# Performance work log

Measured on AMD Instinct MI355X. Metric: run time of the kernel, lower is better.

## Reference

```python
import jax, jax.numpy as jnp
import numpy as np
import math

B, S, D, H, WIN = 2, 4096, 512, 8, 50
DK = D // H


def setup_inputs() -> dict:
    key = jax.random.key(0)
    ks = jax.random.split(key, 10)
    scale = 0.02
    return {
        "x": jax.random.normal(ks[0], (B, S, D), dtype=jnp.float32),
        "opcode_types": jax.random.randint(ks[1], (B, S), 0, 10, dtype=jnp.int64),
        "Wq": jax.random.normal(ks[2], (D, D), dtype=jnp.float32) * scale,
        "bq": jnp.zeros((D,), dtype=jnp.float32),
        "Wk": jax.random.normal(ks[3], (D, D), dtype=jnp.float32) * scale,
        "bk": jnp.zeros((D,), dtype=jnp.float32),
        "Wv": jax.random.normal(ks[4], (D, D), dtype=jnp.float32) * scale,
        "bv": jnp.zeros((D,), dtype=jnp.float32),
        "Wo": jax.random.normal(ks[5], (D, D), dtype=jnp.float32) * scale,
        "bo": jnp.zeros((D,), dtype=jnp.float32),
    }


def reference(x, opcode_types, Wq, bq, Wk, bk, Wv, bv, Wo, bo):
    b, s, d = x.shape
    # Linear projections (torch Linear: x @ W.T + b), split heads -> [B,H,S,DK]
    q = (x @ Wq.T + bq).reshape(b, s, H, DK).transpose(0, 2, 1, 3)
    k = (x @ Wk.T + bk).reshape(b, s, H, DK).transpose(0, 2, 1, 3)
    v = (x @ Wv.T + bv).reshape(b, s, H, DK).transpose(0, 2, 1, 3)

    pos = jnp.arange(s)
    window = jnp.abs(pos[:, None] - pos[None, :]) <= WIN          # [S,S]
    ctrl_cols = (opcode_types == 0).any(axis=0)                   # [S]
    allow = window | ctrl_cols[None, :]                           # [S,S]

    scores = jnp.einsum("bhqd,bhkd->bhqk", q, k) / math.sqrt(DK)  # [B,H,S,S]
    scores = jnp.where(allow[None, None], scores, jnp.float32(-1e9))
    attn = jax.nn.softmax(scores, axis=-1)
    attn = jnp.nan_to_num(attn, nan=0.0)
    out = jnp.einsum("bhqk,bhkd->bhqd", attn, v)                  # [B,H,S,DK]
    out = out.transpose(0, 2, 1, 3).reshape(b, s, d)
    return out @ Wo.T + bo
```

## Files before the change

### kernel.cpp

```cpp
#include <hip/hip_runtime.h>
#include <hip/hip_bf16.h>
#include <math.h>

#define B_ 2
#define S_ 4096
#define D_ 512
#define H_ 8
#define DK_ 64
#define WIN_ 50
#define NGT 32

typedef __attribute__((ext_vector_type(8))) short short8;
typedef __attribute__((ext_vector_type(4))) float f32x4;
typedef __attribute__((ext_vector_type(4))) unsigned short us4;
typedef unsigned short ushort_t;

__device__ __forceinline__ unsigned short f2bf(float f) {
    unsigned u = __builtin_bit_cast(unsigned, f);
    u += 0x7FFF + ((u >> 16) & 1);
    return (unsigned short)(u >> 16);
}
__device__ __forceinline__ float bf2f(unsigned short h) {
    return __builtin_bit_cast(float, ((unsigned)h) << 16);
}
__device__ __forceinline__ unsigned pack_bf16(float lo, float hi) {
    return ((unsigned)f2bf(hi) << 16) | (unsigned)f2bf(lo);
}

__global__ __launch_bounds__(1024) void build_glist(const int* __restrict__ opcode,
                                                    int* __restrict__ glist,
                                                    int* __restrict__ gcount) {
    __shared__ int cnts[1024];
    int t = threadIdx.x;
    int f[4]; int c = 0;
    for (int k = 0; k < 4; ++k) {
        int col = t * 4 + k;
        int flag = 0;
        for (int b = 0; b < B_; ++b) flag |= (opcode[b * S_ + col] == 0) ? 1 : 0;
        f[k] = flag; c += flag;
    }
    cnts[t] = c;
    __syncthreads();
    for (int off = 1; off < 1024; off <<= 1) {
        int v = cnts[t];
        int add = (t >= off) ? cnts[t - off] : 0;
        __syncthreads();
        cnts[t] = v + add;
        __syncthreads();
    }
    int base = cnts[t] - c;
    for (int k = 0; k < 4; ++k) {
        if (f[k]) glist[base++] = t * 4 + k;
    }
    if (t == 1023) gcount[0] = cnts[1023];
}

__global__ __launch_bounds__(256) void split_x(const float* __restrict__ src,
                                               ushort_t* __restrict__ hi,
                                               ushort_t* __restrict__ lo) {
    int i = blockIdx.x * 256 + threadIdx.x;
    f32x4 v = ((const f32x4*)src)[i];
    us4 h, l;
    for (int e = 0; e < 4; ++e) {
        unsigned short hb = f2bf(v[e]);
        h[e] = hb;
        l[e] = f2bf(v[e] - bf2f(hb));
    }
    ((us4*)hi)[i] = h;
    ((us4*)lo)[i] = l;
}

__global__ __launch_bounds__(256) void split_w4(const float* __restrict__ W0, const float* __restrict__ W1,
                                                const float* __restrict__ W2, const float* __restrict__ W3,
                                                ushort_t* __restrict__ H0, ushort_t* __restrict__ H1,
                                                ushort_t* __restrict__ H2, ushort_t* __restrict__ H3,
                                                ushort_t* __restrict__ L0, ushort_t* __restrict__ L1,
                                                ushort_t* __restrict__ L2, ushort_t* __restrict__ L3) {
    const float* src; ushort_t* hp; ushort_t* lp;
    switch (blockIdx.y) {
        case 0: src = W0; hp = H0; lp = L0; break;
        case 1: src = W1; hp = H1; lp = L1; break;
        case 2: src = W2; hp = H2; lp = L2; break;
        default: src = W3; hp = H3; lp = L3; break;
    }
    int i = blockIdx.x * 256 + threadIdx.x;
    f32x4 v = ((const f32x4*)src)[i];
    us4 h, l;
    for (int e = 0; e < 4; ++e) {
        unsigned short hb = f2bf(v[e]);
        h[e] = hb;
        l[e] = f2bf(v[e] - bf2f(hb));
    }
    ((us4*)hp)[i] = h;
    ((us4*)lp)[i] = l;
}

__device__ __forceinline__ void gemm_epi(f32x4 (&acc)[4][4], const float* __restrict__ bias,
                                         void* __restrict__ outp, int mode, float scale,
                                         int m0, int n0, int t) {
    const int lane = t & 63, wave = t >> 6;
    const int lrow = lane & 15, lkg = lane >> 4;
    const int wr = wave >> 1, wc = wave & 1;
    for (int m = 0; m < 4; ++m)
        for (int n = 0; n < 4; ++n) {
            int col = n0 + wc * 64 + n * 16 + lrow;
            int row_base = m0 + wr * 64 + m * 16 + lkg * 4;
            float bs = bias[col];
            float vv[4];
            for (int r = 0; r < 4; ++r) vv[r] = (acc[m][n][r] + bs) * scale;
            if (mode == 0) {
                for (int r = 0; r < 4; ++r)
                    ((float*)outp)[(size_t)(row_base + r) * D_ + col] = vv[r];
            } else if (mode == 1) {
                int bb = row_base >> 12, s0 = row_base & (S_ - 1);
                int hh = col >> 6, dk = col & 63;
                for (int r = 0; r < 4; ++r)
                    ((ushort_t*)outp)[(((size_t)(bb * H_ + hh) * S_) + s0 + r) * DK_ + dk] = f2bf(vv[r]);
            } else if (mode == 2) {
                int bb = row_base >> 12, s0 = row_base & (S_ - 1);
                int hh = col >> 6, dk = col & 63;
                for (int r = 0; r < 4; ++r) {
                    int s = s0 + r, jt = s >> 6, jr = s & 63;
                    char* img = (char*)outp + (((size_t)(bb * H_ + hh)) * 64 + jt) * 16384;
                    *(ushort_t*)(img + ((jr * 128 + dk * 2) ^ ((jr & 7) << 4))) = f2bf(vv[r]);
                }
            } else {
                int bb = row_base >> 12, s0 = row_base & (S_ - 1);
                int hh = col >> 6, dk = col & 63;
                int jt = s0 >> 6, jr0 = s0 & 63;
                char* img = (char*)outp + (((size_t)(bb * H_ + hh)) * 64 + jt) * 16384 + 8192;
                us4 pk;
                for (int r = 0; r < 4; ++r) pk[r] = f2bf(vv[r]);
                *(us4*)(img + ((dk * 128 + jr0 * 2) ^ ((dk & 7) << 4))) = pk;
            }
        }
}

__device__ __forceinline__ void gemm_core1(const ushort_t* __restrict__ A,
                                           const ushort_t* __restrict__ Bw,
                                           ushort_t (&LDS)[2][8192],
                                           int m0, int n0, int t,
                                           f32x4 (&acc)[4][4]) {
    const int lane = t & 63, wave = t >> 6;
    const int lrow = lane & 15, lkg = lane >> 4;
    const int wr = wave >> 1, wc = wave & 1;
    const ushort_t* srcs[2] = {A, Bw};
    const int row0[2] = {m0, n0};

    auto stage = [&](int buf, int k0) {
        #pragma unroll
        for (int it = 0; it < 4; ++it) {
            int c = it * 4 + wave;
            int tile = c >> 3;
            int kg = (c >> 1) & 3;
            int r = ((c & 1) << 6) | lane;
            const ushort_t* g = srcs[tile] + (size_t)(row0[tile] + r) * 512 + k0 + kg * 8;
            __builtin_amdgcn_global_load_lds(
                (const __attribute__((address_space(1))) void*)g,
                (__attribute__((address_space(3))) void*)(&LDS[buf][c * 512]),
                16, 0, 0);
        }
    };

    stage(0, 0);
    __syncthreads();

    const int aoff = lkg * 1024 + (wr * 64 + lrow) * 8;
    const int boff = 4096 + lkg * 1024 + (wc * 64 + lrow) * 8;
    int cur = 0;
    for (int ks = 0; ks < 16; ++ks) {
        if (ks < 15) stage(cur ^ 1, (ks + 1) * 32);
        const ushort_t* Lb = LDS[cur];
        short8 ah[4], bh[4];
        #pragma unroll
        for (int m = 0; m < 4; ++m) ah[m] = *(const short8*)(Lb + aoff + m * 128);
        #pragma unroll
        for (int n = 0; n < 4; ++n) bh[n] = *(const short8*)(Lb + boff + n * 128);
        #pragma unroll
        for (int m = 0; m < 4; ++m)
            #pragma unroll
            for (int n = 0; n < 4; ++n)
                acc[m][n] = __builtin_amdgcn_mfma_f32_16x16x32_bf16(ah[m], bh[n], acc[m][n], 0, 0, 0);
        __syncthreads();
        cur ^= 1;
    }
}

__device__ __forceinline__ void gemm_core3(const ushort_t* __restrict__ Ah,
                                           const ushort_t* __restrict__ Al,
                                           const ushort_t* __restrict__ Bh,
                                           const ushort_t* __restrict__ Bl,
                                           ushort_t (&LDS)[2][16384],
                                           int m0, int n0, int t,
                                           f32x4 (&acc)[4][4]) {
    const int lane = t & 63, wave = t >> 6;
    const int lrow = lane & 15, lkg = lane >> 4;
    const int wr = wave >> 1, wc = wave & 1;
    const ushort_t* srcs[4] = {Ah, Al, Bh, Bl};
    const int row0[4] = {m0, m0, n0, n0};

    auto stage = [&](int buf, int k0) {
        #pragma unroll
        for (int it = 0; it < 8; ++it) {
            int c = it * 4 + wave;
            int tile = c >> 3;
            int kg = (c >> 1) & 3;
            int r = ((c & 1) << 6) | lane;
            const ushort_t* g = srcs[tile] + (size_t)(row0[tile] + r) * 512 + k0 + kg * 8;
            __builtin_amdgcn_global_load_lds(
                (const __attribute__((address_space(1))) void*)g,
                (__attribute__((address_space(3))) void*)(&LDS[buf][c * 512]),
                16, 0, 0);
        }
    };

    stage(0, 0);
    __syncthreads();

    const int aoff = lkg * 1024 + (wr * 64 + lrow) * 8;
    const int boff = 2 * 4096 + lkg * 1024 + (wc * 64 + lrow) * 8;
    int cur = 0;
    for (int ks = 0; ks < 16; ++ks) {
        if (ks < 15) stage(cur ^ 1, (ks + 1) * 32);
        const ushort_t* Lb = LDS[cur];
        short8 ah[4], al[4], bh[4], bl[4];
        #pragma unroll
        for (int m = 0; m < 4; ++m) {
            ah[m] = *(const short8*)(Lb + aoff + m * 128);
            al[m] = *(const short8*)(Lb + 4096 + aoff + m * 128);
        }
        #pragma unroll
        for (int n = 0; n < 4; ++n) {
            bh[n] = *(const short8*)(Lb + boff + n * 128);
            bl[n] = *(const short8*)(Lb + 4096 + boff + n * 128);
        }
        #pragma unroll
        for (int m = 0; m < 4; ++m)
            #pragma unroll
            for (int n = 0; n < 4; ++n) {
                acc[m][n] = __builtin_amdgcn_mfma_f32_16x16x32_bf16(ah[m], bh[n], acc[m][n], 0, 0, 0);
                acc[m][n] = __builtin_amdgcn_mfma_f32_16x16x32_bf16(al[m], bh[n], acc[m][n], 0, 0, 0);
                acc[m][n] = __builtin_amdgcn_mfma_f32_16x16x32_bf16(ah[m], bl[n], acc[m][n], 0, 0, 0);
            }
        __syncthreads();
        cur ^= 1;
    }
}

__global__ __launch_bounds__(256) void gemm_qkv(const ushort_t* __restrict__ xh,
                                                const ushort_t* __restrict__ whb,
                                                const float* __restrict__ bq,
                                                const float* __restrict__ bk,
                                                const float* __restrict__ bv,
                                                ushort_t* __restrict__ qb,
                                                char* __restrict__ bandimg) {
    __shared__ ushort_t LDS[2][8192];
    int z = blockIdx.z;
    const ushort_t* Bh = whb + (size_t)z * D_ * D_;
    const float* bias = (z == 0) ? bq : (z == 1) ? bk : bv;
    int mode = z + 1;
    float scale = (z == 0) ? 0.125f : 1.0f;
    void* outp = (z == 0) ? (void*)qb : (void*)bandimg;
    f32x4 acc[4][4];
    for (int m = 0; m < 4; ++m)
        for (int n = 0; n < 4; ++n)
            acc[m][n] = f32x4{0.f, 0.f, 0.f, 0.f};
    gemm_core1(xh, Bh, LDS, blockIdx.y * 128, blockIdx.x * 128, threadIdx.x, acc);
    gemm_epi(acc, bias, outp, mode, scale, blockIdx.y * 128, blockIdx.x * 128, threadIdx.x);
}

__global__ __launch_bounds__(256) void gemm_fin(const ushort_t* __restrict__ Ah,
                                                const ushort_t* __restrict__ Al,
                                                const ushort_t* __restrict__ Bh,
                                                const ushort_t* __restrict__ Bl,
                                                const float* __restrict__ bias,
                                                float* __restrict__ outp) {
    __shared__ ushort_t LDS[2][16384];
    f32x4 acc[4][4];
    for (int m = 0; m < 4; ++m)
        for (int n = 0; n < 4; ++n)
            acc[m][n] = f32x4{0.f, 0.f, 0.f, 0.f};
    gemm_core3(Ah, Al, Bh, Bl, LDS, blockIdx.y * 128, blockIdx.x * 128, threadIdx.x, acc);
    gemm_epi(acc, bias, (void*)outp, 0, 1.0f, blockIdx.y * 128, blockIdx.x * 128, threadIdx.x);
}

__global__ __launch_bounds__(256) void prep_glob(const char* __restrict__ bandimg,
                                                 char* __restrict__ globimg,
                                                 const int* __restrict__ glist,
                                                 const int* __restrict__ gcount) {
    int G = gcount[0];
    int gc = blockIdx.x;
    if (gc * 64 >= G) return;
    int h = blockIdx.y, b = blockIdx.z;
    int t = threadIdx.x;
    __shared__ int jl[64];
    if (t < 64) { int gi = gc * 64 + t; jl[t] = (gi < G) ? glist[gi] : -1; }
    __syncthreads();
    const size_t bh = (size_t)(b * H_ + h);
    char* dst = globimg + (bh * NGT + gc) * 16384;
    {
        int c = t >> 2, q = t & 3;
        int jj = jl[c];
        #pragma unroll
        for (int p = 0; p < 2; ++p) {
            int o_dst = c * 128 + q * 32 + p * 16;
            short8 val;
            if (jj >= 0) {
                int jr = jj & 63, jt = jj >> 6;
                const char* src = bandimg + (bh * 64 + jt) * 16384;
                val = *(const short8*)(src + ((jr * 128 + q * 32 + p * 16) ^ ((jr & 7) << 4)));
            } else {
                for (int e = 0; e < 8; ++e) val[e] = 0;
            }
            *(short8*)(dst + (o_dst ^ ((c & 7) << 4))) = val;
        }
    }
    {
        int d = t >> 2, qq = t & 3;
        short8 v0, v1;
        #pragma unroll 16
        for (int i = 0; i < 16; ++i) {
            int c = qq * 16 + i;
            int jj = jl[c];
            ushort_t val = 0;
            if (jj >= 0) {
                int jr = jj & 63, jt = jj >> 6;
                const char* src = bandimg + (bh * 64 + jt) * 16384 + 8192;
                val = *(const ushort_t*)(src + ((d * 128 + jr * 2) ^ ((d & 7) << 4)));
            }
            if (i < 8) v0[i] = val; else v1[i - 8] = val;
        }
        int o = d * 128 + qq * 32;
        *(short8*)(dst + 8192 + (o ^ ((d & 7) << 4))) = v0;
        *(short8*)(dst + 8192 + ((o + 16) ^ ((d & 7) << 4))) = v1;
    }
}

__global__ __launch_bounds__(512) void attn_mfma3(const ushort_t* __restrict__ Qp,
                                                  const char* __restrict__ bandimg,
                                                  const char* __restrict__ globimg,
                                                  const int* __restrict__ glist,
                                                  const int* __restrict__ gcount,
                                                  ushort_t* __restrict__ AOh,
                                                  ushort_t* __restrict__ AOl) {
    __shared__ char buf[2][16384];
    __shared__ int jl[2][64];
    __shared__ ushort_t Ps[8 * 16 * 64];

    const int t = threadIdx.x, lane = t & 63, wave = t >> 6;
    const int q = lane & 15, g = lane >> 4;
    const int i0 = blockIdx.x * 128, h = blockIdx.y, b = blockIdx.z;
    const size_t headoff = ((size_t)(b * H_ + h)) * S_ * DK_;
    const int iq = i0 + wave * 16 + q;

    short8 qa[2];
    {
        const ushort_t* qrow = Qp + headoff + (size_t)iq * DK_;
        qa[0] = *(const short8*)(qrow + 8 * g);
        qa[1] = *(const short8*)(qrow + 32 + 8 * g);
    }

    f32x4 Oa[4];
    for (int n = 0; n < 4; ++n) Oa[n] = f32x4{0.f, 0.f, 0.f, 0.f};
    float m_st = -1e30f, l_st = 0.f;

    int jlo = i0 - WIN_;
    int jt_lo = (jlo < 0) ? 0 : (jlo >> 6);
    int jhi = i0 + 127 + WIN_; if (jhi > S_ - 1) jhi = S_ - 1;
    int jt_hi = jhi >> 6;
    int nband = jt_hi - jt_lo + 1;
    const int G = gcount[0];
    int nglob = (G + 63) >> 6; if (nglob > NGT) nglob = NGT;
    int nchunk = nband + nglob;

    const size_t bh = (size_t)(b * H_ + h);

    auto stage = [&](int ch, int nb) {
        const char* img = (ch < nband)
            ? bandimg + (bh * 64 + (jt_lo + ch)) * 16384
            : globimg + (bh * NGT + (ch - nband)) * 16384;
        #pragma unroll
        for (int i = 0; i < 2; ++i) {
            int seg = wave * 2 + i;
            __builtin_amdgcn_global_load_lds(
                (const __attribute__((address_space(1))) void*)(img + seg * 1024 + lane * 16),
                (__attribute__((address_space(3))) void*)(buf[nb] + seg * 1024),
                16, 0, 0);
        }
        if (t < 64) {
            int j;
            if (ch < nband) j = (jt_lo + ch) * 64 + t;
            else { int gi = (ch - nband) * 64 + t; j = (gi < G) ? glist[gi] : -1; }
            jl[nb][t] = j;
        }
    };

    stage(0, 0);
    __syncthreads();

    int cur = 0;
    for (int ch = 0; ch < nchunk; ++ch) {
        if (ch + 1 < nchunk) stage(ch + 1, cur ^ 1);
        const bool isband = ch < nband;
        const char* Kb = buf[cur];
        const char* Vb = buf[cur] + 8192;

        f32x4 sc[4];
        for (int n = 0; n < 4; ++n) sc[n] = f32x4{0.f, 0.f, 0.f, 0.f};
        #pragma unroll
        for (int n = 0; n < 4; ++n) {
            int row = n * 16 + q;
            #pragma unroll
            for (int kt = 0; kt < 2; ++kt) {
                int kb = (row * 128 + g * 16 + kt * 64) ^ ((row & 7) << 4);
                short8 ka = *(const short8*)(Kb + kb);
                sc[n] = __builtin_amdgcn_mfma_f32_16x16x32_bf16(ka, qa[kt], sc[n], 0, 0, 0);
            }
        }

        float pm = -1e30f;
        #pragma unroll
        for (int n = 0; n < 4; ++n) {
            int4 J = *(const int4*)(&jl[cur][n * 16 + g * 4]);
            int js[4] = {J.x, J.y, J.z, J.w};
            #pragma unroll
            for (int r = 0; r < 4; ++r) {
                int jj = js[r];
                int ad = iq - jj; ad = ad < 0 ? -ad : ad;
                bool allow = (jj >= 0) && (isband ? (ad <= WIN_) : (ad > WIN_));
                float s = allow ? sc[n][r] : -1e30f;
                sc[n][r] = s;
                pm = fmaxf(pm, s);
            }
        }
        pm = fmaxf(pm, __shfl_xor(pm, 16, 64));
        pm = fmaxf(pm, __shfl_xor(pm, 32, 64));

        bool skip = __all(pm <= m_st);
        float fac = 1.0f;
        if (!skip) {
            float mn = fmaxf(m_st, pm);
            fac = __expf(m_st - mn);
            m_st = mn;
        }
        float rs = 0.f;
        #pragma unroll
        for (int n = 0; n < 4; ++n)
            #pragma unroll
            for (int r = 0; r < 4; ++r) {
                float p = __expf(sc[n][r] - m_st);
                sc[n][r] = p;
                rs += p;
            }
        rs += __shfl_xor(rs, 16, 64);
        rs += __shfl_xor(rs, 32, 64);
        l_st = skip ? (l_st + rs) : (l_st * fac + rs);

        ushort_t* Pw = Ps + wave * 1024;
        #pragma unroll
        for (int n = 0; n < 4; ++n)
            #pragma unroll
            for (int hh = 0; hh < 2; ++hh) {
                unsigned pk = pack_bf16(sc[n][2 * hh], sc[n][2 * hh + 1]);
                int off = (q * 128 + n * 32 + g * 8 + hh * 4) ^ ((q & 7) << 4);
                *(unsigned*)((char*)Pw + off) = pk;
            }

        if (!skip) {
            #pragma unroll
            for (int n = 0; n < 4; ++n)
                #pragma unroll
                for (int r = 0; r < 4; ++r) Oa[n][r] *= fac;
        }

        short8 pa[2];
        #pragma unroll
        for (int kt = 0; kt < 2; ++kt) {
            int pb = (q * 128 + g * 16 + kt * 64) ^ ((q & 7) << 4);
            pa[kt] = *(const short8*)((char*)Pw + pb);
        }
        #pragma unroll
        for (int n = 0; n < 4; ++n) {
            int row = n * 16 + q;
            #pragma unroll
            for (int kt = 0; kt < 2; ++kt) {
                int vb = (row * 128 + g * 16 + kt * 64) ^ ((row & 7) << 4);
                short8 va = *(const short8*)(Vb + vb);
                Oa[n] = __builtin_amdgcn_mfma_f32_16x16x32_bf16(va, pa[kt], Oa[n], 0, 0, 0);
            }
        }
        __syncthreads();
        cur ^= 1;
    }

    float inv = 1.0f / l_st;
    #pragma unroll
    for (int n = 0; n < 4; ++n) {
        us4 ph, pl;
        #pragma unroll
        for (int r = 0; r < 4; ++r) {
            float v = Oa[n][r] * inv;
            unsigned short hb = f2bf(v);
            ph[r] = hb;
            pl[r] = f2bf(v - bf2f(hb));
        }
        size_t base = ((size_t)b * S_ + iq) * D_ + h * DK_ + (n * 16 + g * 4);
        *(us4*)(AOh + base) = ph;
        *(us4*)(AOl + base) = pl;
    }
}

extern "C" void kernel_launch(void* const* d_in, const int* in_sizes, int n_in,
                              void* d_out, int out_size, void* d_ws, size_t ws_size,
                              hipStream_t stream) {
    const float* x      = (const float*)d_in[0];
    const int*   opcode = (const int*)d_in[1];
    const float* Wq = (const float*)d_in[2];
    const float* bq = (const float*)d_in[3];
    const float* Wk = (const float*)d_in[4];
    const float* bk = (const float*)d_in[5];
    const float* Wv = (const float*)d_in[6];
    const float* bv = (const float*)d_in[7];
    const float* Wo = (const float*)d_in[8];
    const float* bo = (const float*)d_in[9];
    float* out = (float*)d_out;

    char* ws = (char*)d_ws;
    const size_t bsd = (size_t)B_ * S_ * D_;
    const size_t bf_bytes = bsd * sizeof(ushort_t);
    const size_t w_bytes  = (size_t)D_ * D_ * sizeof(ushort_t);

    ushort_t* qb = (ushort_t*)(ws);
    ushort_t* xh = (ushort_t*)(ws + bf_bytes);
    ushort_t* xl = (ushort_t*)(ws + 2 * bf_bytes);
    ushort_t* aoh = xh;
    ushort_t* aol = xl;
    char* wbase = ws + 3 * bf_bytes;
    ushort_t* Wh[4]; ushort_t* Wl[4];
    for (int i = 0; i < 4; ++i) {
        Wh[i] = (ushort_t*)(wbase + i * w_bytes);
        Wl[i] = (ushort_t*)(wbase + (4 + i) * w_bytes);
    }
    char* bandimg = wbase + 8 * w_bytes;
    char* globimg = bandimg + (size_t)16 * 64 * 16384;
    int* glist  = (int*)(globimg + (size_t)16 * NGT * 16384);
    int* gcount = glist + S_;

    build_glist<<<1, 1024, 0, stream>>>(opcode, glist, gcount);
    split_x<<<(int)(bsd / 4 / 256), 256, 0, stream>>>(x, xh, xl);
    split_w4<<<dim3(D_ * D_ / 4 / 256, 4), 256, 0, stream>>>(Wq, Wk, Wv, Wo,
        Wh[0], Wh[1], Wh[2], Wh[3], Wl[0], Wl[1], Wl[2], Wl[3]);

    gemm_qkv<<<dim3(D_ / 128, (B_ * S_) / 128, 3), 256, 0, stream>>>(
        xh, Wh[0], bq, bk, bv, qb, bandimg);

    prep_glob<<<dim3(NGT, H_, B_), 256, 0, stream>>>(bandimg, globimg, glist, gcount);

    attn_mfma3<<<dim3(S_ / 128, H_, B_), 512, 0, stream>>>(
        qb, bandimg, globimg, glist, gcount, aoh, aol);

    gemm_fin<<<dim3(D_ / 128, (B_ * S_) / 128), 256, 0, stream>>>(
        aoh, aol, Wh[3], Wl[3], bo, out);
}
```

Baseline: 218.5 us.

## Fuse prep kernels, transpose GEMM epilogues, use exp2 softmax and precomputed LDS offsets

Three preprocessing kernels (glist build, x split, weight split) merge into one launch, and the unused x-lo and Q/K/V-lo splits are dropped. The Q and K GEMMs and the output GEMM are transposed (weights as the A operand) so the epilogues write vectorized us4/f32x4 stores. Q is prescaled by log2(e)/8 so attention can use exp2f. The attention kernel precomputes swizzled LDS offsets, computes band masks arithmetically instead of loading a j-list, and packs P with v_cvt_pk_bf16. The aim is to cut launch overhead, preprocessing traffic and ALU work, at the cost of more code complexity and possible epilogue layout bugs.

```diff
diff --git a/kernel.cpp b/kernel.cpp
--- a/kernel.cpp
+++ b/kernel.cpp
@@ -9,6 +9,7 @@
 #define DK_ 64
 #define WIN_ 50
 #define NGT 32
+#define QSCALE 0.18033688011112042f
 
 typedef __attribute__((ext_vector_type(8))) short short8;
 typedef __attribute__((ext_vector_type(4))) float f32x4;
@@ -23,117 +24,67 @@
 __device__ __forceinline__ float bf2f(unsigned short h) {
     return __builtin_bit_cast(float, ((unsigned)h) << 16);
 }
-__device__ __forceinline__ unsigned pack_bf16(float lo, float hi) {
-    return ((unsigned)f2bf(hi) << 16) | (unsigned)f2bf(lo);
-}
-
-__global__ __launch_bounds__(1024) void build_glist(const int* __restrict__ opcode,
-                                                    int* __restrict__ glist,
-                                                    int* __restrict__ gcount) {
-    __shared__ int cnts[1024];
-    int t = threadIdx.x;
-    int f[4]; int c = 0;
-    for (int k = 0; k < 4; ++k) {
-        int col = t * 4 + k;
-        int flag = 0;
-        for (int b = 0; b < B_; ++b) flag |= (opcode[b * S_ + col] == 0) ? 1 : 0;
-        f[k] = flag; c += flag;
-    }
-    cnts[t] = c;
-    __syncthreads();
-    for (int off = 1; off < 1024; off <<= 1) {
-        int v = cnts[t];
-        int add = (t >= off) ? cnts[t - off] : 0;
+__device__ __forceinline__ unsigned cvt_pk_bf16(float lo, float hi) {
+    unsigned r;
+    asm("v_cvt_pk_bf16_f32 %0, %1, %2" : "=v"(r) : "v"(lo), "v"(hi));
+    return r;
+}
+
+__global__ __launch_bounds__(256) void prep_all(const float* __restrict__ x,
+                                                const float* __restrict__ W0,
+                                                const float* __restrict__ W1,
+                                                const float* __restrict__ W2,
+                                                const float* __restrict__ W3,
+                                                const int* __restrict__ opcode,
+                                                ushort_t* __restrict__ xh,
+                                                ushort_t* __restrict__ whb,
+                                                ushort_t* __restrict__ wol,
+                                                int* __restrict__ glist,
+                                                int* __restrict__ gcount) {
+    const int bid = blockIdx.x;
+    const int t = threadIdx.x;
+    if (bid < 4096) {
+        int i = bid * 256 + t;
+        f32x4 v = ((const f32x4*)x)[i];
+        us4 hv;
+        for (int e = 0; e < 4; ++e) hv[e] = f2bf(v[e]);
+        ((us4*)xh)[i] = hv;
+    } else if (bid < 5120) {
+        int b2 = bid - 4096;
+        int wz = b2 >> 8, inner = b2 & 255;
+        const float* src = (wz == 0) ? W0 : (wz == 1) ? W1 : (wz == 2) ? W2 : W3;
+        int i = inner * 256 + t;
+        f32x4 v = ((const f32x4*)src)[i];
+        us4 hv, lv;
+        for (int e = 0; e < 4; ++e) {
+            unsigned short hb = f2bf(v[e]);
+            hv[e] = hb;
+            lv[e] = f2bf(v[e] - bf2f(hb));
+        }
+        ((us4*)(whb + (size_t)wz * D_ * D_))[i] = hv;
+        if (wz == 3) ((us4*)wol)[i] = lv;
+    } else {
+        __shared__ int cnts[256];
+        unsigned fl = 0; int c = 0;
+        for (int k = 0; k < 16; ++k) {
+            int col = t * 16 + k;
+            int flag = (opcode[col] == 0) | (opcode[S_ + col] == 0);
+            fl |= (unsigned)flag << k; c += flag;
+        }
+        cnts[t] = c;
         __syncthreads();
-        cnts[t] = v + add;
-        __syncthreads();
-    }
-    int base = cnts[t] - c;
-    for (int k = 0; k < 4; ++k) {
-        if (f[k]) glist[base++] = t * 4 + k;
-    }
-    if (t == 1023) gcount[0] = cnts[1023];
-}
-
-__global__ __launch_bounds__(256) void split_x(const float* __restrict__ src,
-                                               ushort_t* __restrict__ hi,
-                                               ushort_t* __restrict__ lo) {
-    int i = blockIdx.x * 256 + threadIdx.x;
-    f32x4 v = ((const f32x4*)src)[i];
-    us4 h, l;
-    for (int e = 0; e < 4; ++e) {
-        unsigned short hb = f2bf(v[e]);
-        h[e] = hb;
-        l[e] = f2bf(v[e] - bf2f(hb));
-    }
-    ((us4*)hi)[i] = h;
-    ((us4*)lo)[i] = l;
-}
-
-__global__ __launch_bounds__(256) void split_w4(const float* __restrict__ W0, const float* __restrict__ W1,
-                                                const float* __restrict__ W2, const float* __restrict__ W3,
-                                                ushort_t* __restrict__ H0, ushort_t* __restrict__ H1,
-                                                ushort_t* __restrict__ H2, ushort_t* __restrict__ H3,
-                                                ushort_t* __restrict__ L0, ushort_t* __restrict__ L1,
-                                                ushort_t* __restrict__ L2, ushort_t* __restrict__ L3) {
-    const float* src; ushort_t* hp; ushort_t* lp;
-    switch (blockIdx.y) {
-        case 0: src = W0; hp = H0; lp = L0; break;
-        case 1: src = W1; hp = H1; lp = L1; break;
-        case 2: src = W2; hp = H2; lp = L2; break;
-        default: src = W3; hp = H3; lp = L3; break;
-    }
-    int i = blockIdx.x * 256 + threadIdx.x;
-    f32x4 v = ((const f32x4*)src)[i];
-    us4 h, l;
-    for (int e = 0; e < 4; ++e) {
-        unsigned short hb = f2bf(v[e]);
-        h[e] = hb;
-        l[e] = f2bf(v[e] - bf2f(hb));
-    }
-    ((us4*)hp)[i] = h;
-    ((us4*)lp)[i] = l;
-}
-
-__device__ __forceinline__ void gemm_epi(f32x4 (&acc)[4][4], const float* __restrict__ bias,
-                                         void* __restrict__ outp, int mode, float scale,
-                                         int m0, int n0, int t) {
-    const int lane = t & 63, wave = t >> 6;
-    const int lrow = lane & 15, lkg = lane >> 4;
-    const int wr = wave >> 1, wc = wave & 1;
-    for (int m = 0; m < 4; ++m)
-        for (int n = 0; n < 4; ++n) {
-            int col = n0 + wc * 64 + n * 16 + lrow;
-            int row_base = m0 + wr * 64 + m * 16 + lkg * 4;
-            float bs = bias[col];
-            float vv[4];
-            for (int r = 0; r < 4; ++r) vv[r] = (acc[m][n][r] + bs) * scale;
-            if (mode == 0) {
-                for (int r = 0; r < 4; ++r)
-                    ((float*)outp)[(size_t)(row_base + r) * D_ + col] = vv[r];
-            } else if (mode == 1) {
-                int bb = row_base >> 12, s0 = row_base & (S_ - 1);
-                int hh = col >> 6, dk = col & 63;
-                for (int r = 0; r < 4; ++r)
-                    ((ushort_t*)outp)[(((size_t)(bb * H_ + hh) * S_) + s0 + r) * DK_ + dk] = f2bf(vv[r]);
-            } else if (mode == 2) {
-                int bb = row_base >> 12, s0 = row_base & (S_ - 1);
-                int hh = col >> 6, dk = col & 63;
-                for (int r = 0; r < 4; ++r) {
-                    int s = s0 + r, jt = s >> 6, jr = s & 63;
-                    char* img = (char*)outp + (((size_t)(bb * H_ + hh)) * 64 + jt) * 16384;
-                    *(ushort_t*)(img + ((jr * 128 + dk * 2) ^ ((jr & 7) << 4))) = f2bf(vv[r]);
-                }
-            } else {
-                int bb = row_base >> 12, s0 = row_base & (S_ - 1);
-                int hh = col >> 6, dk = col & 63;
-                int jt = s0 >> 6, jr0 = s0 & 63;
-                char* img = (char*)outp + (((size_t)(bb * H_ + hh)) * 64 + jt) * 16384 + 8192;
-                us4 pk;
-                for (int r = 0; r < 4; ++r) pk[r] = f2bf(vv[r]);
-                *(us4*)(img + ((dk * 128 + jr0 * 2) ^ ((dk & 7) << 4))) = pk;
-            }
-        }
+        for (int off = 1; off < 256; off <<= 1) {
+            int v = cnts[t];
+            int a = (t >= off) ? cnts[t - off] : 0;
+            __syncthreads();
+            cnts[t] = v + a;
+            __syncthreads();
+        }
+        int base = cnts[t] - c;
+        for (int k = 0; k < 16; ++k)
+            if ((fl >> k) & 1) glist[base++] = t * 16 + k;
+        if (t == 255) gcount[0] = cnts[255];
+    }
 }
 
 __device__ __forceinline__ void gemm_core1(const ushort_t* __restrict__ A,
@@ -255,33 +206,90 @@
                                                 ushort_t* __restrict__ qb,
                                                 char* __restrict__ bandimg) {
     __shared__ ushort_t LDS[2][8192];
-    int z = blockIdx.z;
-    const ushort_t* Bh = whb + (size_t)z * D_ * D_;
-    const float* bias = (z == 0) ? bq : (z == 1) ? bk : bv;
-    int mode = z + 1;
-    float scale = (z == 0) ? 0.125f : 1.0f;
-    void* outp = (z == 0) ? (void*)qb : (void*)bandimg;
+    const int z = blockIdx.z;
+    const int t = threadIdx.x;
+    const ushort_t* Wz = whb + (size_t)z * D_ * D_;
+    const int lane = t & 63, wave = t >> 6;
+    const int lrow = lane & 15, lkg = lane >> 4;
+    const int wr = wave >> 1, wc = wave & 1;
+
     f32x4 acc[4][4];
     for (int m = 0; m < 4; ++m)
         for (int n = 0; n < 4; ++n)
             acc[m][n] = f32x4{0.f, 0.f, 0.f, 0.f};
-    gemm_core1(xh, Bh, LDS, blockIdx.y * 128, blockIdx.x * 128, threadIdx.x, acc);
-    gemm_epi(acc, bias, outp, mode, scale, blockIdx.y * 128, blockIdx.x * 128, threadIdx.x);
-}
-
-__global__ __launch_bounds__(256) void gemm_fin(const ushort_t* __restrict__ Ah,
-                                                const ushort_t* __restrict__ Al,
-                                                const ushort_t* __restrict__ Bh,
-                                                const ushort_t* __restrict__ Bl,
+
+    if (z == 2) {
+        const int m0 = blockIdx.y * 128, n0 = blockIdx.x * 128;
+        gemm_core1(xh, Wz, LDS, m0, n0, t, acc);
+        for (int m = 0; m < 4; ++m) {
+            int s_base = m0 + wr * 64 + m * 16 + lkg * 4;
+            int bb = s_base >> 12, s0 = s_base & (S_ - 1);
+            int jt = s0 >> 6, jr0 = s0 & 63;
+            for (int n = 0; n < 4; ++n) {
+                int col = n0 + wc * 64 + n * 16 + lrow;
+                float bs = bv[col];
+                int hh = col >> 6, dk = col & 63;
+                us4 pk;
+                for (int r = 0; r < 4; ++r) pk[r] = f2bf(acc[m][n][r] + bs);
+                char* img = bandimg + (((size_t)(bb * H_ + hh)) * 64 + jt) * 16384 + 8192;
+                *(us4*)(img + ((dk * 128 + jr0 * 2) ^ ((dk & 7) << 4))) = pk;
+            }
+        }
+    } else {
+        const int m0 = blockIdx.x * 128, n0 = blockIdx.y * 128;
+        gemm_core1(Wz, xh, LDS, m0, n0, t, acc);
+        const float* bias = (z == 0) ? bq : bk;
+        for (int m = 0; m < 4; ++m) {
+            int d_base = m0 + wr * 64 + m * 16 + lkg * 4;
+            f32x4 b4 = *(const f32x4*)(bias + d_base);
+            int hh = d_base >> 6, dkb = d_base & 63;
+            for (int n = 0; n < 4; ++n) {
+                int s = n0 + wc * 64 + n * 16 + lrow;
+                int bb = s >> 12, sl = s & (S_ - 1);
+                us4 pk;
+                if (z == 0) {
+                    for (int r = 0; r < 4; ++r) pk[r] = f2bf((acc[m][n][r] + b4[r]) * QSCALE);
+                    *(us4*)(qb + (((size_t)(bb * H_ + hh) * S_) + sl) * DK_ + dkb) = pk;
+                } else {
+                    for (int r = 0; r < 4; ++r) pk[r] = f2bf(acc[m][n][r] + b4[r]);
+                    int jt = sl >> 6, jr = sl & 63;
+                    char* img = bandimg + (((size_t)(bb * H_ + hh)) * 64 + jt) * 16384;
+                    *(us4*)(img + ((jr * 128 + dkb * 2) ^ ((jr & 7) << 4))) = pk;
+                }
+            }
+        }
+    }
+}
+
+__global__ __launch_bounds__(256) void gemm_fin(const ushort_t* __restrict__ Woh,
+                                                const ushort_t* __restrict__ Wol,
+                                                const ushort_t* __restrict__ aoh,
+                                                const ushort_t* __restrict__ aol,
                                                 const float* __restrict__ bias,
                                                 float* __restrict__ outp) {
     __shared__ ushort_t LDS[2][16384];
+    const int t = threadIdx.x;
+    const int lane = t & 63, wave = t >> 6;
+    const int lrow = lane & 15, lkg = lane >> 4;
+    const int wr = wave >> 1, wc = wave & 1;
+    const int m0 = blockIdx.x * 128, n0 = blockIdx.y * 128;
+
     f32x4 acc[4][4];
     for (int m = 0; m < 4; ++m)
         for (int n = 0; n < 4; ++n)
             acc[m][n] = f32x4{0.f, 0.f, 0.f, 0.f};
-    gemm_core3(Ah, Al, Bh, Bl, LDS, blockIdx.y * 128, blockIdx.x * 128, threadIdx.x, acc);
-    gemm_epi(acc, bias, (void*)outp, 0, 1.0f, blockIdx.y * 128, blockIdx.x * 128, threadIdx.x);
+    gemm_core3(Woh, Wol, aoh, aol, LDS, m0, n0, t, acc);
+
+    for (int m = 0; m < 4; ++m) {
+        int d_base = m0 + wr * 64 + m * 16 + lkg * 4;
+        f32x4 b4 = *(const f32x4*)(bias + d_base);
+        for (int n = 0; n < 4; ++n) {
+            int s = n0 + wc * 64 + n * 16 + lrow;
+            f32x4 o;
+            for (int r = 0; r < 4; ++r) o[r] = acc[m][n][r] + b4[r];
+            *(f32x4*)(outp + (size_t)s * D_ + d_base) = o;
+        }
+    }
 }
 
 __global__ __launch_bounds__(256) void prep_glob(const char* __restrict__ bandimg,
@@ -336,7 +344,7 @@
     }
 }
 
-__global__ __launch_bounds__(512) void attn_mfma3(const ushort_t* __restrict__ Qp,
+__global__ __launch_bounds__(512) void attn_mfma4(const ushort_t* __restrict__ Qp,
                                                   const char* __restrict__ bandimg,
                                                   const char* __restrict__ globimg,
                                                   const int* __restrict__ glist,
@@ -352,6 +360,7 @@
     const int i0 = blockIdx.x * 128, h = blockIdx.y, b = blockIdx.z;
     const size_t headoff = ((size_t)(b * H_ + h)) * S_ * DK_;
     const int iq = i0 + wave * 16 + q;
+    const int iqm = iq - WIN_;
 
     short8 qa[2];
     {
@@ -375,6 +384,19 @@
 
     const size_t bh = (size_t)(b * H_ + h);
 
+    int koff[4][2], poffw[4], poffr[2];
+    #pragma unroll
+    for (int n = 0; n < 4; ++n) {
+        int row = n * 16 + q;
+        #pragma unroll
+        for (int kt = 0; kt < 2; ++kt)
+            koff[n][kt] = (row * 128 + g * 16 + kt * 64) ^ ((row & 7) << 4);
+        poffw[n] = (q * 128 + n * 32 + g * 8) ^ ((q & 7) << 4);
+    }
+    #pragma unroll
+    for (int kt = 0; kt < 2; ++kt)
+        poffr[kt] = (q * 128 + g * 16 + kt * 64) ^ ((q & 7) << 4);
+
     auto stage = [&](int ch, int nb) {
         const char* img = (ch < nband)
             ? bandimg + (bh * 64 + (jt_lo + ch)) * 16384
@@ -387,11 +409,9 @@
                 (__attribute__((address_space(3))) void*)(buf[nb] + seg * 1024),
                 16, 0, 0);
         }
-        if (t < 64) {
-            int j;
-            if (ch < nband) j = (jt_lo + ch) * 64 + t;
-            else { int gi = (ch - nband) * 64 + t; j = (gi < G) ? glist[gi] : -1; }
-            jl[nb][t] = j;
+        if (ch >= nband && t < 64) {
+            int gi = (ch - nband) * 64 + t;
+            jl[nb][t] = (gi < G) ? glist[gi] : -1;
         }
     };
 
@@ -402,35 +422,47 @@
     for (int ch = 0; ch < nchunk; ++ch) {
         if (ch + 1 < nchunk) stage(ch + 1, cur ^ 1);
         const bool isband = ch < nband;
+        const int cbase = isband ? (jt_lo + ch) * 64 : 0;
         const char* Kb = buf[cur];
         const char* Vb = buf[cur] + 8192;
 
         f32x4 sc[4];
         for (int n = 0; n < 4; ++n) sc[n] = f32x4{0.f, 0.f, 0.f, 0.f};
         #pragma unroll
-        for (int n = 0; n < 4; ++n) {
-            int row = n * 16 + q;
+        for (int n = 0; n < 4; ++n)
             #pragma unroll
             for (int kt = 0; kt < 2; ++kt) {
-                int kb = (row * 128 + g * 16 + kt * 64) ^ ((row & 7) << 4);
-                short8 ka = *(const short8*)(Kb + kb);
+                short8 ka = *(const short8*)(Kb + koff[n][kt]);
                 sc[n] = __builtin_amdgcn_mfma_f32_16x16x32_bf16(ka, qa[kt], sc[n], 0, 0, 0);
             }
-        }
 
         float pm = -1e30f;
-        #pragma unroll
-        for (int n = 0; n < 4; ++n) {
-            int4 J = *(const int4*)(&jl[cur][n * 16 + g * 4]);
-            int js[4] = {J.x, J.y, J.z, J.w};
-            #pragma unroll
-            for (int r = 0; r < 4; ++r) {
-                int jj = js[r];
-                int ad = iq - jj; ad = ad < 0 ? -ad : ad;
-                bool allow = (jj >= 0) && (isband ? (ad <= WIN_) : (ad > WIN_));
-                float s = allow ? sc[n][r] : -1e30f;
-                sc[n][r] = s;
-                pm = fmaxf(pm, s);
+        if (isband) {
+            #pragma unroll
+            for (int n = 0; n < 4; ++n) {
+                int jb = cbase + n * 16 + 4 * g;
+                #pragma unroll
+                for (int r = 0; r < 4; ++r) {
+                    bool inwin = (unsigned)(jb + r - iqm) <= 2 * WIN_;
+                    float s = inwin ? sc[n][r] : -1e30f;
+                    sc[n][r] = s;
+                    pm = fmaxf(pm, s);
+                }
+            }
+        } else {
+            #pragma unroll
+            for (int n = 0; n < 4; ++n) {
+                int4 J = *(const int4*)(&jl[cur][n * 16 + g * 4]);
+                int js[4] = {J.x, J.y, J.z, J.w};
+                #pragma unroll
+                for (int r = 0; r < 4; ++r) {
+                    int jj = js[r];
+                    bool inwin = (unsigned)(jj - iqm) <= 2 * WIN_;
+                    bool allow = (jj >= 0) && !inwin;
+                    float s = allow ? sc[n][r] : -1e30f;
+                    sc[n][r] = s;
+                    pm = fmaxf(pm, s);
+                }
             }
         }
         pm = fmaxf(pm, __shfl_xor(pm, 16, 64));
@@ -440,7 +472,7 @@
         float fac = 1.0f;
         if (!skip) {
             float mn = fmaxf(m_st, pm);
-            fac = __expf(m_st - mn);
+            fac = exp2f(m_st - mn);
             m_st = mn;
         }
         float rs = 0.f;
@@ -448,7 +480,7 @@
         for (int n = 0; n < 4; ++n)
             #pragma unroll
             for (int r = 0; r < 4; ++r) {
-                float p = __expf(sc[n][r] - m_st);
+                float p = exp2f(sc[n][r] - m_st);
                 sc[n][r] = p;
                 rs += p;
             }
@@ -458,13 +490,12 @@
 
         ushort_t* Pw = Ps + wave * 1024;
         #pragma unroll
-        for (int n = 0; n < 4; ++n)
-            #pragma unroll
-            for (int hh = 0; hh < 2; ++hh) {
-                unsigned pk = pack_bf16(sc[n][2 * hh], sc[n][2 * hh + 1]);
-                int off = (q * 128 + n * 32 + g * 8 + hh * 4) ^ ((q & 7) << 4);
-                *(unsigned*)((char*)Pw + off) = pk;
-            }
+        for (int n = 0; n < 4; ++n) {
+            unsigned pk0 = cvt_pk_bf16(sc[n][0], sc[n][1]);
+            unsigned pk1 = cvt_pk_bf16(sc[n][2], sc[n][3]);
+            *(unsigned long long*)((char*)Pw + poffw[n]) =
+                ((unsigned long long)pk1 << 32) | pk0;
+        }
 
         if (!skip) {
             #pragma unroll
@@ -475,20 +506,15 @@
 
         short8 pa[2];
         #pragma unroll
-        for (int kt = 0; kt < 2; ++kt) {
-            int pb = (q * 128 + g * 16 + kt * 64) ^ ((q & 7) << 4);
-            pa[kt] = *(const short8*)((char*)Pw + pb);
-        }
-        #pragma unroll
-        for (int n = 0; n < 4; ++n) {
-            int row = n * 16 + q;
+        for (int kt = 0; kt < 2; ++kt)
+            pa[kt] = *(const short8*)((char*)Pw + poffr[kt]);
+        #pragma unroll
+        for (int n = 0; n < 4; ++n)
             #pragma unroll
             for (int kt = 0; kt < 2; ++kt) {
-                int vb = (row * 128 + g * 16 + kt * 64) ^ ((row & 7) << 4);
-                short8 va = *(const short8*)(Vb + vb);
+                short8 va = *(const short8*)(Vb + koff[n][kt]);
                 Oa[n] = __builtin_amdgcn_mfma_f32_16x16x32_bf16(va, pa[kt], Oa[n], 0, 0, 0);
             }
-        }
         __syncthreads();
         cur ^= 1;
     }
@@ -530,35 +556,29 @@
     const size_t bf_bytes = bsd * sizeof(ushort_t);
     const size_t w_bytes  = (size_t)D_ * D_ * sizeof(ushort_t);
 
-    ushort_t* qb = (ushort_t*)(ws);
-    ushort_t* xh = (ushort_t*)(ws + bf_bytes);
-    ushort_t* xl = (ushort_t*)(ws + 2 * bf_bytes);
+    ushort_t* qb  = (ushort_t*)(ws);
+    ushort_t* xh  = (ushort_t*)(ws + bf_bytes);
+    ushort_t* aol = (ushort_t*)(ws + 2 * bf_bytes);
     ushort_t* aoh = xh;
-    ushort_t* aol = xl;
     char* wbase = ws + 3 * bf_bytes;
-    ushort_t* Wh[4]; ushort_t* Wl[4];
-    for (int i = 0; i < 4; ++i) {
-        Wh[i] = (ushort_t*)(wbase + i * w_bytes);
-        Wl[i] = (ushort_t*)(wbase + (4 + i) * w_bytes);
-    }
-    char* bandimg = wbase + 8 * w_bytes;
+    ushort_t* whb = (ushort_t*)wbase;
+    ushort_t* wol = (ushort_t*)(wbase + 4 * w_bytes);
+    char* bandimg = wbase + 5 * w_bytes;
     char* globimg = bandimg + (size_t)16 * 64 * 16384;
     int* glist  = (int*)(globimg + (size_t)16 * NGT * 16384);
     int* gcount = glist + S_;
 
-    build_glist<<<1, 1024, 0, stream>>>(opcode, glist, gcount);
-    split_x<<<(int)(bsd / 4 / 256), 256, 0, stream>>>(x, xh, xl);
-    split_w4<<<dim3(D_ * D_ / 4 / 256, 4), 256, 0, stream>>>(Wq, Wk, Wv, Wo,
-        Wh[0], Wh[1], Wh[2], Wh[3], Wl[0], Wl[1], Wl[2], Wl[3]);
+    prep_all<<<5121, 256, 0, stream>>>(x, Wq, Wk, Wv, Wo, opcode,
+                                       xh, whb, wol, glist, gcount);
 
     gemm_qkv<<<dim3(D_ / 128, (B_ * S_) / 128, 3), 256, 0, stream>>>(
-        xh, Wh[0], bq, bk, bv, qb, bandimg);
+        xh, whb, bq, bk, bv, qb, bandimg);
 
     prep_glob<<<dim3(NGT, H_, B_), 256, 0, stream>>>(bandimg, globimg, glist, gcount);
 
-    attn_mfma3<<<dim3(S_ / 128, H_, B_), 512, 0, stream>>>(
+    attn_mfma4<<<dim3(S_ / 128, H_, B_), 512, 0, stream>>>(
         qb, bandimg, globimg, glist, gcount, aoh, aol);
 
     gemm_fin<<<dim3(D_ / 128, (B_ * S_) / 128), 256, 0, stream>>>(
-        aoh, aol, Wh[3], Wl[3], bo, out);
-}
+        whb + 3 * (size_t)D_ * D_, wol, aoh, aol, bo, out);
+}
```

Result: faster. 204.7 us (-6.3%).
